# Performance work log

Hardware: AMD Instinct MI355X
Metric: run time of the kernel (lower is better)

## Reference

```python
import jax, jax.numpy as jnp
import numpy as np

INPUT_SIZE = 64
OUTPUT_SIZE = 64
HIDDEN = 1024
SAMPLES = 32
STEPS = 128


def _forward(inputs, W_in, b_in, W_ih0, W_hh0, b_ih0, b_hh0,
             W_ih1, W_hh1, b_ih1, b_hh1, W_out, b_out):
    # Faithful to the torch module: per outer step, inputs[:, step, :].unsqueeze(1)
    # is fed to a batch_first=False LSTM, so the sample axis acts as time (batch=1)
    # and hidden state carries across steps -> equivalent to ONE batch-1 LSTM over
    # the step-major flattened sequence of length steps*samples.
    # Dropout (p=0.05 between LSTM layers) is treated as eval-mode (identity).
    S, steps, D = inputs.shape
    H = W_in.shape[0]
    x = jnp.transpose(inputs, (1, 0, 2)).reshape(steps * S, D)  # (T, D), step-major
    z = x @ W_in.T + b_in                                        # input Linear (T, H)
    # layer-0 input contributions precomputed over all time (big GEMM)
    pre0 = z @ W_ih0.T + (b_ih0 + b_hh0)                         # (T, 4H)
    b1 = b_ih1 + b_hh1

    def step(carry, p0):
        h0, c0, h1, c1 = carry
        g0 = p0 + W_hh0 @ h0                                      # (4H,)
        i0, f0, gg0, o0 = jnp.split(g0, 4)
        c0 = jax.nn.sigmoid(f0) * c0 + jax.nn.sigmoid(i0) * jnp.tanh(gg0)
        h0 = jax.nn.sigmoid(o0) * jnp.tanh(c0)
        g1 = W_ih1 @ h0 + W_hh1 @ h1 + b1
        i1, f1, gg1, o1 = jnp.split(g1, 4)
        c1 = jax.nn.sigmoid(f1) * c1 + jax.nn.sigmoid(i1) * jnp.tanh(gg1)
        h1 = jax.nn.sigmoid(o1) * jnp.tanh(c1)
        return (h0, c0, h1, c1), h1

    zero = jnp.zeros((H,), inputs.dtype)
    (_, _, _, _), hs = jax.lax.scan(step, (zero, zero, zero, zero), pre0)  # hs: (T, H)
    y = hs @ W_out.T + b_out                                     # output Linear (T, out)
    return jnp.transpose(y.reshape(steps, S, -1), (1, 0, 2))     # (samples, steps, out)


def setup_inputs() -> dict:
    key = jax.random.key(0)
    ks = jax.random.split(key, 16)
    H, D, O = HIDDEN, INPUT_SIZE, OUTPUT_SIZE
    s = 1.0 / np.sqrt(H)
    u = lambda k, shape: jax.random.uniform(k, shape, jnp.float32, -s, s)
    return {
        "inputs": jax.random.normal(ks[0], (SAMPLES, STEPS, D), jnp.float32),
        "W_in": u(ks[1], (H, D)),
        "b_in": u(ks[2], (H,)),
        "W_ih0": u(ks[3], (4 * H, H)),
        "W_hh0": u(ks[4], (4 * H, H)),
        "b_ih0": u(ks[5], (4 * H,)),
        "b_hh0": u(ks[6], (4 * H,)),
        "W_ih1": u(ks[7], (4 * H, H)),
        "W_hh1": u(ks[8], (4 * H, H)),
        "b_ih1": u(ks[9], (4 * H,)),
        "b_hh1": u(ks[10], (4 * H,)),
        "W_out": u(ks[11], (O, H)),
        "b_out": u(ks[12], (O,)),
    }


def reference(inputs, W_in, b_in, W_ih0, W_hh0, b_ih0, b_hh0,
              W_ih1, W_hh1, b_ih1, b_hh1, W_out, b_out):
    return _forward(inputs, W_in, b_in, W_ih0, W_hh0, b_ih0, b_hh0,
                    W_ih1, W_hh1, b_ih1, b_hh1, W_out, b_out)
```

## Files before the change

kernel.cpp:

```cpp
#include <hip/hip_runtime.h>
#include <math.h>


#define T_STEPS 4096
#define HID 1024
#define UPB 8
#define NBLK 256

typedef unsigned long long u64;

#define AGENT_LD64(p) __hip_atomic_load((p), __ATOMIC_RELAXED, __HIP_MEMORY_SCOPE_AGENT)
#define AGENT_ST64(p, v) __hip_atomic_store((p), (v), __ATOMIC_RELAXED, __HIP_MEMORY_SCOPE_AGENT)

__device__ __forceinline__ u64 pack_h(float h, int tag) {
  return (u64)__float_as_uint(h) | ((u64)(unsigned)tag << 32);
}
__device__ __forceinline__ float pkt_val(u64 v) { return __uint_as_float((unsigned)v); }
__device__ __forceinline__ int pkt_tag(u64 v) { return (int)(v >> 32); }

__device__ __forceinline__ float fast_sigm(float x) {
  return __builtin_amdgcn_rcpf(1.f + __expf(-x));
}
__device__ __forceinline__ float fast_tanh(float x) {
  return 2.f * __builtin_amdgcn_rcpf(1.f + __expf(-2.f * x)) - 1.f;
}

__device__ __forceinline__ void pace_wait(u64 t_last, u64 per) {
  if (per) {
    u64 target = t_last + (per >> 1) + (per >> 4);
    while ((long long)(__builtin_amdgcn_s_memrealtime() - target) < 0)
      __builtin_amdgcn_s_sleep(2);
  }
}
__device__ __forceinline__ void pace_update(u64* t_last, u64* per) {
  u64 now = __builtin_amdgcn_s_memrealtime();
  if (*t_last) {
    u64 d = now - *t_last;
    if (d > 1024) d = 1024;
    *per = *per ? ((*per * 3 + d) >> 2) : d;
  }
  *t_last = now;
}

__global__ void k_clear(u64* __restrict__ p, long n) {
  long i = (long)blockIdx.x * blockDim.x + threadIdx.x;
  long stride = (long)gridDim.x * blockDim.x;
  for (; i < n; i += stride) p[i] = 0ULL;
}

__global__ void k_prep(const float* __restrict__ inputs,
                       const float* __restrict__ b_ih0, const float* __restrict__ b_hh0,
                       const float* __restrict__ b_ih1, const float* __restrict__ b_hh1,
                       float* __restrict__ xg, float* __restrict__ bsum0,
                       float* __restrict__ b1sum) {
  int i = blockIdx.x * 256 + threadIdx.x;
  if (i < T_STEPS * 64) {
    int t = i >> 6, d = i & 63;
    xg[i] = inputs[(t & 31) * 8192 + (t >> 5) * 64 + d];
  }
  if (i < 4096) {
    bsum0[i] = b_ih0[i] + b_hh0[i];
    b1sum[i] = b_ih1[i] + b_hh1[i];
  }
}

__global__ __launch_bounds__(256) void gemm_nt(
    const float* __restrict__ A, const float* __restrict__ B,
    const float* __restrict__ bias, float* __restrict__ C,
    int M, int N, int K, int mode) {
  __shared__ float As[8][128];
  __shared__ float Bs[8][128];
  const int tid = threadIdx.x;
  const int bm = blockIdx.x * 128;
  const int bn = blockIdx.y * 128;
  const int tm = tid >> 4;
  const int tn = tid & 15;
  const int lr = tid >> 1;
  const int lk = (tid & 1) * 4;

  float acc[8][8];
#pragma unroll
  for (int i = 0; i < 8; i++)
#pragma unroll
    for (int j = 0; j < 8; j++) acc[i][j] = 0.f;

  const float* Ap = A + (long)(bm + lr) * K + lk;
  const bool bvalid = (bn + lr) < N;
  const float* Bp = B + (long)(bvalid ? (bn + lr) : 0) * K + lk;

  for (int k0 = 0; k0 < K; k0 += 8) {
    float4 av = *(const float4*)(Ap + k0);
    float4 bv = bvalid ? *(const float4*)(Bp + k0) : make_float4(0.f, 0.f, 0.f, 0.f);
    As[lk + 0][lr] = av.x; As[lk + 1][lr] = av.y;
    As[lk + 2][lr] = av.z; As[lk + 3][lr] = av.w;
    Bs[lk + 0][lr] = bv.x; Bs[lk + 1][lr] = bv.y;
    Bs[lk + 2][lr] = bv.z; Bs[lk + 3][lr] = bv.w;
    __syncthreads();
#pragma unroll
    for (int kk = 0; kk < 8; kk++) {
      float a[8], b[8];
      *(float4*)&a[0] = *(const float4*)&As[kk][tm * 8];
      *(float4*)&a[4] = *(const float4*)&As[kk][tm * 8 + 4];
      *(float4*)&b[0] = *(const float4*)&Bs[kk][tn * 8];
      *(float4*)&b[4] = *(const float4*)&Bs[kk][tn * 8 + 4];
#pragma unroll
      for (int i = 0; i < 8; i++)
#pragma unroll
        for (int j = 0; j < 8; j++) acc[i][j] = fmaf(a[i], b[j], acc[i][j]);
    }
    __syncthreads();
  }

  const int n0 = bn + tn * 8;
  if (n0 < N) {
    float bb[8];
#pragma unroll
    for (int j = 0; j < 8; j++) bb[j] = bias[n0 + j];
#pragma unroll
    for (int i = 0; i < 8; i++) {
      int m = bm + tm * 8 + i;
      float4 v0, v1;
      v0.x = acc[i][0] + bb[0]; v0.y = acc[i][1] + bb[1];
      v0.z = acc[i][2] + bb[2]; v0.w = acc[i][3] + bb[3];
      v1.x = acc[i][4] + bb[4]; v1.y = acc[i][5] + bb[5];
      v1.z = acc[i][6] + bb[6]; v1.w = acc[i][7] + bb[7];
      if (mode == 0) {
        long o = (long)m * N + n0;
        *(float4*)&C[o] = v0; *(float4*)&C[o + 4] = v1;
      } else {
        long o = (long)(m & 31) * 8192 + (long)(m >> 5) * 64 + n0;
        *(float4*)&C[o] = v0; *(float4*)&C[o + 4] = v1;
      }
    }
  }
}

__global__ __launch_bounds__(1024, 1) void lstm_fused(
    const float* __restrict__ pre0,
    const float* __restrict__ Whh0,
    const float* __restrict__ Wih1,
    const float* __restrict__ Whh1,
    const float* __restrict__ b1sum,
    u64* __restrict__ pk0,
    u64* __restrict__ pk1,
    float* __restrict__ h1_hist) {
  __shared__ float ha_lds[HID];
  __shared__ float hb_lds[HID];
  __shared__ float scr[32];
  __shared__ float pre_lds[32];
  const int b = blockIdx.x;
  const int tid = threadIdx.x;
  const int wave = tid >> 6;
  const int lane = tid & 63;

  if (b < 128) {
    const int j0 = b * UPB;
    float w0[16], w1[16];
    {
      int r0 = 2 * wave, r1 = 2 * wave + 1;
      const float* s0 = Whh0 + (long)((r0 >> 3) * HID + j0 + (r0 & 7)) * HID + lane;
      const float* s1 = Whh0 + (long)((r1 >> 3) * HID + j0 + (r1 & 7)) * HID + lane;
#pragma unroll
      for (int m = 0; m < 16; m++) { w0[m] = s0[m << 6]; w1[m] = s1[m << 6]; }
    }
    float c_state = 0.f;
    u64 t_last = 0, per = 0;
    __syncthreads();

    for (int t = 0; t < T_STEPS; t++) {
      float preval = 0.f;
      if (tid < 32)
        preval = pre0[(long)t * 4096 + ((tid >> 3) << 10) + j0 + (tid & 7)];

      if (t > 0) {
        const u64* p = pk0 + (long)(t - 1) * HID + tid;
        pace_wait(t_last, per);
        u64 v;
        for (;;) {
          v = AGENT_LD64(p);
          if (pkt_tag(v) == t) break;
          __builtin_amdgcn_s_sleep(1);
        }
        pace_update(&t_last, &per);
        ha_lds[tid] = pkt_val(v);
      } else {
        ha_lds[tid] = 0.f;
      }
      if (tid < 32) pre_lds[tid] = preval;
      __syncthreads();

      float s0 = 0.f, s1 = 0.f;
#pragma unroll
      for (int m = 0; m < 16; m++) {
        float hv = ha_lds[lane + (m << 6)];
        s0 = fmaf(w0[m], hv, s0);
        s1 = fmaf(w1[m], hv, s1);
      }
#pragma unroll
      for (int off = 32; off >= 1; off >>= 1) {
        s0 += __shfl_xor(s0, off, 64);
        s1 += __shfl_xor(s1, off, 64);
      }
      if (lane == 0) { scr[wave * 2] = s0; scr[wave * 2 + 1] = s1; }
      __syncthreads();

      if (tid < UPB) {
        float gi = scr[tid]      + pre_lds[tid];
        float gf = scr[8 + tid]  + pre_lds[8 + tid];
        float gg = scr[16 + tid] + pre_lds[16 + tid];
        float go = scr[24 + tid] + pre_lds[24 + tid];
        c_state = fast_sigm(gf) * c_state + fast_sigm(gi) * fast_tanh(gg);
        float h = fast_sigm(go) * fast_tanh(c_state);
        AGENT_ST64(&pk0[(long)t * HID + j0 + tid], pack_h(h, t + 1));
      }
    }
  } else {
    const int j0 = (b - 128) * UPB;
    float wi0[16], wi1[16], wh0[16], wh1[16];
    {
      int r0 = 2 * wave, r1 = 2 * wave + 1;
      long o0 = (long)((r0 >> 3) * HID + j0 + (r0 & 7)) * HID + lane;
      long o1 = (long)((r1 >> 3) * HID + j0 + (r1 & 7)) * HID + lane;
      const float* a0 = Wih1 + o0; const float* a1 = Wih1 + o1;
      const float* c0 = Whh1 + o0; const float* c1 = Whh1 + o1;
#pragma unroll
      for (int m = 0; m < 16; m++) {
        wi0[m] = a0[m << 6]; wi1[m] = a1[m << 6];
        wh0[m] = c0[m << 6]; wh1[m] = c1[m << 6];
      }
    }
    if (tid < 32)
      pre_lds[tid] = b1sum[((tid >> 3) << 10) + j0 + (tid & 7)];
    float c_state = 0.f;
    u64 t_last = 0, per = 0;
    __syncthreads();

    for (int r = 1; r <= T_STEPS; r++) {
      const u64* p0 = pk0 + (long)(r - 1) * HID + tid;
      const u64* p1 = pk1 + (long)((r >= 2) ? (r - 2) : 0) * HID + tid;
      pace_wait(t_last, per);
      u64 v0 = 0, v1 = 0;
      bool ok0 = false, ok1 = (r < 2);
      for (;;) {
        if (!ok0) { v0 = AGENT_LD64(p0); ok0 = (pkt_tag(v0) == r); }
        if (!ok1) { v1 = AGENT_LD64(p1); ok1 = (pkt_tag(v1) == r - 1); }
        if (ok0 && ok1) break;
        __builtin_amdgcn_s_sleep(1);
      }
      pace_update(&t_last, &per);
      ha_lds[tid] = pkt_val(v0);
      hb_lds[tid] = (r >= 2) ? pkt_val(v1) : 0.f;
      __syncthreads();

      float s0 = 0.f, s1 = 0.f;
#pragma unroll
      for (int m = 0; m < 16; m++) {
        float av = ha_lds[lane + (m << 6)];
        float bv = hb_lds[lane + (m << 6)];
        s0 = fmaf(wi0[m], av, s0);
        s0 = fmaf(wh0[m], bv, s0);
        s1 = fmaf(wi1[m], av, s1);
        s1 = fmaf(wh1[m], bv, s1);
      }
#pragma unroll
      for (int off = 32; off >= 1; off >>= 1) {
        s0 += __shfl_xor(s0, off, 64);
        s1 += __shfl_xor(s1, off, 64);
      }
      if (lane == 0) { scr[wave * 2] = s0; scr[wave * 2 + 1] = s1; }
      __syncthreads();

      if (tid < UPB) {
        float gi = scr[tid]      + pre_lds[tid];
        float gf = scr[8 + tid]  + pre_lds[8 + tid];
        float gg = scr[16 + tid] + pre_lds[16 + tid];
        float go = scr[24 + tid] + pre_lds[24 + tid];
        c_state = fast_sigm(gf) * c_state + fast_sigm(gi) * fast_tanh(gg);
        float h = fast_sigm(go) * fast_tanh(c_state);
        AGENT_ST64(&pk1[(long)(r - 1) * HID + j0 + tid], pack_h(h, r));
        h1_hist[(long)(r - 1) * HID + j0 + tid] = h;
      }
    }
  }
}

extern "C" void kernel_launch(void* const* d_in, const int* in_sizes, int n_in,
                              void* d_out, int out_size, void* d_ws, size_t ws_size,
                              hipStream_t stream) {
  const float* inputs = (const float*)d_in[0];
  const float* W_in  = (const float*)d_in[1];
  const float* b_in  = (const float*)d_in[2];
  const float* W_ih0 = (const float*)d_in[3];
  const float* W_hh0 = (const float*)d_in[4];
  const float* b_ih0 = (const float*)d_in[5];
  const float* b_hh0 = (const float*)d_in[6];
  const float* W_ih1 = (const float*)d_in[7];
  const float* W_hh1 = (const float*)d_in[8];
  const float* b_ih1 = (const float*)d_in[9];
  const float* b_hh1 = (const float*)d_in[10];
  const float* W_out = (const float*)d_in[11];
  const float* b_out = (const float*)d_in[12];
  float* out = (float*)d_out;

  char* ws = (char*)d_ws;
  float* pre_big = (float*)(ws);
  u64*   pk0     = (u64*)  (ws + ((size_t)64 << 20));
  u64*   pk1     = (u64*)  (ws + ((size_t)96 << 20));
  float* zbuf    = (float*)(ws + ((size_t)128 << 20));
  float* xg      = (float*)(ws + ((size_t)144 << 20));
  float* bsum0   = (float*)(ws + ((size_t)145 << 20));
  float* b1sum   = (float*)(ws + ((size_t)145 << 20) + 16384);

  k_clear<<<2048, 256, 0, stream>>>(pk0, (long)2 * T_STEPS * HID);
  k_prep<<<1024, 256, 0, stream>>>(inputs, b_ih0, b_hh0, b_ih1, b_hh1,
                                   xg, bsum0, b1sum);
  gemm_nt<<<dim3(32, 8), 256, 0, stream>>>(xg, W_in, b_in, zbuf,
                                           T_STEPS, HID, 64, 0);
  gemm_nt<<<dim3(32, 32), 256, 0, stream>>>(zbuf, W_ih0, bsum0, pre_big,
                                            T_STEPS, 4096, HID, 0);
  lstm_fused<<<NBLK, 1024, 0, stream>>>(pre_big, W_hh0, W_ih1, W_hh1, b1sum,
                                        pk0, pk1, zbuf);
  gemm_nt<<<dim3(32, 1), 256, 0, stream>>>(zbuf, W_out, b_out, out,
                                           T_STEPS, 64, HID, 1);
}
```

Before: 10.27 ms.

## Remap LSTM recurrence to one hidden unit per wave with single barrier per step

Result: slower. 18.13 ms (+76.6%).

```diff
diff --git a/kernel.cpp b/kernel.cpp
--- a/kernel.cpp
+++ b/kernel.cpp
@@ -27,7 +27,7 @@
 
 __device__ __forceinline__ void pace_wait(u64 t_last, u64 per) {
   if (per) {
-    u64 target = t_last + (per >> 1) + (per >> 4);
+    u64 target = t_last + (per >> 2) + (per >> 3);
     while ((long long)(__builtin_amdgcn_s_memrealtime() - target) < 0)
       __builtin_amdgcn_s_sleep(2);
   }
@@ -135,7 +135,7 @@
   }
 }
 
-__global__ __launch_bounds__(1024, 1) void lstm_fused(
+__global__ __launch_bounds__(512) void lstm_fused(
     const float* __restrict__ pre0,
     const float* __restrict__ Whh0,
     const float* __restrict__ Wih1,
@@ -144,141 +144,164 @@
     u64* __restrict__ pk0,
     u64* __restrict__ pk1,
     float* __restrict__ h1_hist) {
-  __shared__ float ha_lds[HID];
-  __shared__ float hb_lds[HID];
-  __shared__ float scr[32];
-  __shared__ float pre_lds[32];
+  __shared__ float ha[2][HID];
+  __shared__ float hb[2][HID];
   const int b = blockIdx.x;
   const int tid = threadIdx.x;
   const int wave = tid >> 6;
   const int lane = tid & 63;
 
   if (b < 128) {
-    const int j0 = b * UPB;
-    float w0[16], w1[16];
-    {
-      int r0 = 2 * wave, r1 = 2 * wave + 1;
-      const float* s0 = Whh0 + (long)((r0 >> 3) * HID + j0 + (r0 & 7)) * HID + lane;
-      const float* s1 = Whh0 + (long)((r1 >> 3) * HID + j0 + (r1 & 7)) * HID + lane;
-#pragma unroll
-      for (int m = 0; m < 16; m++) { w0[m] = s0[m << 6]; w1[m] = s1[m << 6]; }
-    }
+    const int u = b * UPB + wave;
+    float4 wgt[4][4];
+#pragma unroll
+    for (int g = 0; g < 4; g++)
+#pragma unroll
+      for (int q = 0; q < 4; q++)
+        wgt[g][q] = *(const float4*)(Whh0 + ((long)((g << 10) + u) << 10) +
+                                     (q << 8) + (lane << 2));
     float c_state = 0.f;
     u64 t_last = 0, per = 0;
-    __syncthreads();
 
     for (int t = 0; t < T_STEPS; t++) {
       float preval = 0.f;
-      if (tid < 32)
-        preval = pre0[(long)t * 4096 + ((tid >> 3) << 10) + j0 + (tid & 7)];
+      if (lane < 4) preval = pre0[(long)t * 4096 + (lane << 10) + u];
+      const int par = t & 1;
 
       if (t > 0) {
-        const u64* p = pk0 + (long)(t - 1) * HID + tid;
+        const u64* p = pk0 + (long)(t - 1) * HID + 2 * tid;
         pace_wait(t_last, per);
-        u64 v;
+        u64 v0, v1;
         for (;;) {
-          v = AGENT_LD64(p);
-          if (pkt_tag(v) == t) break;
+          v0 = AGENT_LD64(p); v1 = AGENT_LD64(p + 1);
+          if (pkt_tag(v0) == t && pkt_tag(v1) == t) break;
           __builtin_amdgcn_s_sleep(1);
         }
         pace_update(&t_last, &per);
-        ha_lds[tid] = pkt_val(v);
+        *(float2*)&ha[par][2 * tid] = make_float2(pkt_val(v0), pkt_val(v1));
       } else {
-        ha_lds[tid] = 0.f;
-      }
-      if (tid < 32) pre_lds[tid] = preval;
+        *(float2*)&ha[par][2 * tid] = make_float2(0.f, 0.f);
+      }
       __syncthreads();
 
-      float s0 = 0.f, s1 = 0.f;
-#pragma unroll
-      for (int m = 0; m < 16; m++) {
-        float hv = ha_lds[lane + (m << 6)];
-        s0 = fmaf(w0[m], hv, s0);
-        s1 = fmaf(w1[m], hv, s1);
+      float s0 = 0.f, s1 = 0.f, s2 = 0.f, s3 = 0.f;
+#pragma unroll
+      for (int q = 0; q < 4; q++) {
+        float4 hv = *(const float4*)&ha[par][(q << 8) + (lane << 2)];
+        s0 = fmaf(wgt[0][q].x, hv.x, s0); s0 = fmaf(wgt[0][q].y, hv.y, s0);
+        s0 = fmaf(wgt[0][q].z, hv.z, s0); s0 = fmaf(wgt[0][q].w, hv.w, s0);
+        s1 = fmaf(wgt[1][q].x, hv.x, s1); s1 = fmaf(wgt[1][q].y, hv.y, s1);
+        s1 = fmaf(wgt[1][q].z, hv.z, s1); s1 = fmaf(wgt[1][q].w, hv.w, s1);
+        s2 = fmaf(wgt[2][q].x, hv.x, s2); s2 = fmaf(wgt[2][q].y, hv.y, s2);
+        s2 = fmaf(wgt[2][q].z, hv.z, s2); s2 = fmaf(wgt[2][q].w, hv.w, s2);
+        s3 = fmaf(wgt[3][q].x, hv.x, s3); s3 = fmaf(wgt[3][q].y, hv.y, s3);
+        s3 = fmaf(wgt[3][q].z, hv.z, s3); s3 = fmaf(wgt[3][q].w, hv.w, s3);
       }
 #pragma unroll
       for (int off = 32; off >= 1; off >>= 1) {
-        s0 += __shfl_xor(s0, off, 64);
-        s1 += __shfl_xor(s1, off, 64);
-      }
-      if (lane == 0) { scr[wave * 2] = s0; scr[wave * 2 + 1] = s1; }
-      __syncthreads();
-
-      if (tid < UPB) {
-        float gi = scr[tid]      + pre_lds[tid];
-        float gf = scr[8 + tid]  + pre_lds[8 + tid];
-        float gg = scr[16 + tid] + pre_lds[16 + tid];
-        float go = scr[24 + tid] + pre_lds[24 + tid];
-        c_state = fast_sigm(gf) * c_state + fast_sigm(gi) * fast_tanh(gg);
-        float h = fast_sigm(go) * fast_tanh(c_state);
-        AGENT_ST64(&pk0[(long)t * HID + j0 + tid], pack_h(h, t + 1));
+        s0 += __shfl_xor(s0, off, 64); s1 += __shfl_xor(s1, off, 64);
+        s2 += __shfl_xor(s2, off, 64); s3 += __shfl_xor(s3, off, 64);
+      }
+      float act = 0.f;
+      if (lane < 4) {
+        float sel = (lane == 0) ? s0 : (lane == 1) ? s1 : (lane == 2) ? s2 : s3;
+        sel += preval;
+        act = (lane == 2) ? fast_tanh(sel) : fast_sigm(sel);
+      }
+      float af = __shfl(act, 1, 64);
+      float ag = __shfl(act, 2, 64);
+      float ao = __shfl(act, 3, 64);
+      if (lane == 0) {
+        c_state = af * c_state + act * ag;
+        float h = ao * fast_tanh(c_state);
+        AGENT_ST64(&pk0[(long)t * HID + u], pack_h(h, t + 1));
       }
     }
   } else {
-    const int j0 = (b - 128) * UPB;
-    float wi0[16], wi1[16], wh0[16], wh1[16];
-    {
-      int r0 = 2 * wave, r1 = 2 * wave + 1;
-      long o0 = (long)((r0 >> 3) * HID + j0 + (r0 & 7)) * HID + lane;
-      long o1 = (long)((r1 >> 3) * HID + j0 + (r1 & 7)) * HID + lane;
-      const float* a0 = Wih1 + o0; const float* a1 = Wih1 + o1;
-      const float* c0 = Whh1 + o0; const float* c1 = Whh1 + o1;
-#pragma unroll
-      for (int m = 0; m < 16; m++) {
-        wi0[m] = a0[m << 6]; wi1[m] = a1[m << 6];
-        wh0[m] = c0[m << 6]; wh1[m] = c1[m << 6];
-      }
-    }
-    if (tid < 32)
-      pre_lds[tid] = b1sum[((tid >> 3) << 10) + j0 + (tid & 7)];
+    const int u = (b - 128) * UPB + wave;
+    float4 wi[4][4], wh[4][4];
+#pragma unroll
+    for (int g = 0; g < 4; g++)
+#pragma unroll
+      for (int q = 0; q < 4; q++) {
+        long o = ((long)((g << 10) + u) << 10) + (q << 8) + (lane << 2);
+        wi[g][q] = *(const float4*)(Wih1 + o);
+        wh[g][q] = *(const float4*)(Whh1 + o);
+      }
+    float preval = 0.f;
+    if (lane < 4) preval = b1sum[(lane << 10) + u];
     float c_state = 0.f;
     u64 t_last = 0, per = 0;
-    __syncthreads();
 
     for (int r = 1; r <= T_STEPS; r++) {
-      const u64* p0 = pk0 + (long)(r - 1) * HID + tid;
-      const u64* p1 = pk1 + (long)((r >= 2) ? (r - 2) : 0) * HID + tid;
+      const int par = r & 1;
+      const u64* p0 = pk0 + (long)(r - 1) * HID + 2 * tid;
+      const u64* p1 = pk1 + (long)((r >= 2) ? (r - 2) : 0) * HID + 2 * tid;
       pace_wait(t_last, per);
-      u64 v0 = 0, v1 = 0;
-      bool ok0 = false, ok1 = (r < 2);
-      for (;;) {
-        if (!ok0) { v0 = AGENT_LD64(p0); ok0 = (pkt_tag(v0) == r); }
-        if (!ok1) { v1 = AGENT_LD64(p1); ok1 = (pkt_tag(v1) == r - 1); }
-        if (ok0 && ok1) break;
-        __builtin_amdgcn_s_sleep(1);
+      u64 a0, a1, b0 = 0, b1 = 0;
+      if (r >= 2) {
+        for (;;) {
+          a0 = AGENT_LD64(p0); a1 = AGENT_LD64(p0 + 1);
+          b0 = AGENT_LD64(p1); b1 = AGENT_LD64(p1 + 1);
+          if (pkt_tag(a0) == r && pkt_tag(a1) == r &&
+              pkt_tag(b0) == r - 1 && pkt_tag(b1) == r - 1) break;
+          __builtin_amdgcn_s_sleep(1);
+        }
+      } else {
+        for (;;) {
+          a0 = AGENT_LD64(p0); a1 = AGENT_LD64(p0 + 1);
+          if (pkt_tag(a0) == r && pkt_tag(a1) == r) break;
+          __builtin_amdgcn_s_sleep(1);
+        }
       }
       pace_update(&t_last, &per);
-      ha_lds[tid] = pkt_val(v0);
-      hb_lds[tid] = (r >= 2) ? pkt_val(v1) : 0.f;
+      *(float2*)&ha[par][2 * tid] = make_float2(pkt_val(a0), pkt_val(a1));
+      *(float2*)&hb[par][2 * tid] = (r >= 2)
+          ? make_float2(pkt_val(b0), pkt_val(b1))
+          : make_float2(0.f, 0.f);
       __syncthreads();
 
-      float s0 = 0.f, s1 = 0.f;
-#pragma unroll
-      for (int m = 0; m < 16; m++) {
-        float av = ha_lds[lane + (m << 6)];
-        float bv = hb_lds[lane + (m << 6)];
-        s0 = fmaf(wi0[m], av, s0);
-        s0 = fmaf(wh0[m], bv, s0);
-        s1 = fmaf(wi1[m], av, s1);
-        s1 = fmaf(wh1[m], bv, s1);
+      float s0 = 0.f, s1 = 0.f, s2 = 0.f, s3 = 0.f;
+#pragma unroll
+      for (int q = 0; q < 4; q++) {
+        float4 va = *(const float4*)&ha[par][(q << 8) + (lane << 2)];
+        float4 vb = *(const float4*)&hb[par][(q << 8) + (lane << 2)];
+        s0 = fmaf(wi[0][q].x, va.x, s0); s0 = fmaf(wi[0][q].y, va.y, s0);
+        s0 = fmaf(wi[0][q].z, va.z, s0); s0 = fmaf(wi[0][q].w, va.w, s0);
+        s0 = fmaf(wh[0][q].x, vb.x, s0); s0 = fmaf(wh[0][q].y, vb.y, s0);
+        s0 = fmaf(wh[0][q].z, vb.z, s0); s0 = fmaf(wh[0][q].w, vb.w, s0);
+        s1 = fmaf(wi[1][q].x, va.x, s1); s1 = fmaf(wi[1][q].y, va.y, s1);
+        s1 = fmaf(wi[1][q].z, va.z, s1); s1 = fmaf(wi[1][q].w, va.w, s1);
+        s1 = fmaf(wh[1][q].x, vb.x, s1); s1 = fmaf(wh[1][q].y, vb.y, s1);
+        s1 = fmaf(wh[1][q].z, vb.z, s1); s1 = fmaf(wh[1][q].w, vb.w, s1);
+        s2 = fmaf(wi[2][q].x, va.x, s2); s2 = fmaf(wi[2][q].y, va.y, s2);
+        s2 = fmaf(wi[2][q].z, va.z, s2); s2 = fmaf(wi[2][q].w, va.w, s2);
+        s2 = fmaf(wh[2][q].x, vb.x, s2); s2 = fmaf(wh[2][q].y, vb.y, s2);
+        s2 = fmaf(wh[2][q].z, vb.z, s2); s2 = fmaf(wh[2][q].w, vb.w, s2);
+        s3 = fmaf(wi[3][q].x, va.x, s3); s3 = fmaf(wi[3][q].y, va.y, s3);
+        s3 = fmaf(wi[3][q].z, va.z, s3); s3 = fmaf(wi[3][q].w, va.w, s3);
+        s3 = fmaf(wh[3][q].x, vb.x, s3); s3 = fmaf(wh[3][q].y, vb.y, s3);
+        s3 = fmaf(wh[3][q].z, vb.z, s3); s3 = fmaf(wh[3][q].w, vb.w, s3);
       }
 #pragma unroll
       for (int off = 32; off >= 1; off >>= 1) {
-        s0 += __shfl_xor(s0, off, 64);
-        s1 += __shfl_xor(s1, off, 64);
-      }
-      if (lane == 0) { scr[wave * 2] = s0; scr[wave * 2 + 1] = s1; }
-      __syncthreads();
-
-      if (tid < UPB) {
-        float gi = scr[tid]      + pre_lds[tid];
-        float gf = scr[8 + tid]  + pre_lds[8 + tid];
-        float gg = scr[16 + tid] + pre_lds[16 + tid];
-        float go = scr[24 + tid] + pre_lds[24 + tid];
-        c_state = fast_sigm(gf) * c_state + fast_sigm(gi) * fast_tanh(gg);
-        float h = fast_sigm(go) * fast_tanh(c_state);
-        AGENT_ST64(&pk1[(long)(r - 1) * HID + j0 + tid], pack_h(h, r));
-        h1_hist[(long)(r - 1) * HID + j0 + tid] = h;
+        s0 += __shfl_xor(s0, off, 64); s1 += __shfl_xor(s1, off, 64);
+        s2 += __shfl_xor(s2, off, 64); s3 += __shfl_xor(s3, off, 64);
+      }
+      float act = 0.f;
+      if (lane < 4) {
+        float sel = (lane == 0) ? s0 : (lane == 1) ? s1 : (lane == 2) ? s2 : s3;
+        sel += preval;
+        act = (lane == 2) ? fast_tanh(sel) : fast_sigm(sel);
+      }
+      float af = __shfl(act, 1, 64);
+      float ag = __shfl(act, 2, 64);
+      float ao = __shfl(act, 3, 64);
+      if (lane == 0) {
+        c_state = af * c_state + act * ag;
+        float h = ao * fast_tanh(c_state);
+        AGENT_ST64(&pk1[(long)(r - 1) * HID + u], pack_h(h, r));
+        h1_hist[(long)(r - 1) * HID + u] = h;
       }
     }
   }
@@ -318,8 +341,8 @@
                                            T_STEPS, HID, 64, 0);
   gemm_nt<<<dim3(32, 32), 256, 0, stream>>>(zbuf, W_ih0, bsum0, pre_big,
                                             T_STEPS, 4096, HID, 0);
-  lstm_fused<<<NBLK, 1024, 0, stream>>>(pre_big, W_hh0, W_ih1, W_hh1, b1sum,
-                                        pk0, pk1, zbuf);
+  lstm_fused<<<NBLK, 512, 0, stream>>>(pre_big, W_hh0, W_ih1, W_hh1, b1sum,
+                                       pk0, pk1, zbuf);
   gemm_nt<<<dim3(32, 1), 256, 0, stream>>>(zbuf, W_out, b_out, out,
                                            T_STEPS, 64, HID, 1);
 }
```

## Merge both LSTM layers into every block with 4 units per block

Applied to the files above, without the earlier changes.

Result: slower. 16.68 ms (+62.5%).

```diff
diff --git a/kernel.cpp b/kernel.cpp
--- a/kernel.cpp
+++ b/kernel.cpp
@@ -4,7 +4,7 @@
 
 #define T_STEPS 4096
 #define HID 1024
-#define UPB 8
+#define UPB 4
 #define NBLK 256
 
 typedef unsigned long long u64;
@@ -27,7 +27,7 @@
 
 __device__ __forceinline__ void pace_wait(u64 t_last, u64 per) {
   if (per) {
-    u64 target = t_last + (per >> 1) + (per >> 4);
+    u64 target = t_last + (per >> 1);
     while ((long long)(__builtin_amdgcn_s_memrealtime() - target) < 0)
       __builtin_amdgcn_s_sleep(2);
   }
@@ -135,7 +135,7 @@
   }
 }
 
-__global__ __launch_bounds__(1024, 1) void lstm_fused(
+__global__ __launch_bounds__(1024) void lstm_fused(
     const float* __restrict__ pre0,
     const float* __restrict__ Whh0,
     const float* __restrict__ Wih1,
@@ -144,141 +144,135 @@
     u64* __restrict__ pk0,
     u64* __restrict__ pk1,
     float* __restrict__ h1_hist) {
-  __shared__ float ha_lds[HID];
-  __shared__ float hb_lds[HID];
-  __shared__ float scr[32];
-  __shared__ float pre_lds[32];
+  __shared__ float ha[2][HID];
+  __shared__ float hb[2][HID];
+  __shared__ float scr0[4][16];
+  __shared__ float scr1[4][16];
   const int b = blockIdx.x;
   const int tid = threadIdx.x;
   const int wave = tid >> 6;
   const int lane = tid & 63;
-
-  if (b < 128) {
-    const int j0 = b * UPB;
-    float w0[16], w1[16];
-    {
-      int r0 = 2 * wave, r1 = 2 * wave + 1;
-      const float* s0 = Whh0 + (long)((r0 >> 3) * HID + j0 + (r0 & 7)) * HID + lane;
-      const float* s1 = Whh0 + (long)((r1 >> 3) * HID + j0 + (r1 & 7)) * HID + lane;
-#pragma unroll
-      for (int m = 0; m < 16; m++) { w0[m] = s0[m << 6]; w1[m] = s1[m << 6]; }
-    }
-    float c_state = 0.f;
-    u64 t_last = 0, per = 0;
-    __syncthreads();
-
-    for (int t = 0; t < T_STEPS; t++) {
-      float preval = 0.f;
-      if (tid < 32)
-        preval = pre0[(long)t * 4096 + ((tid >> 3) << 10) + j0 + (tid & 7)];
-
-      if (t > 0) {
-        const u64* p = pk0 + (long)(t - 1) * HID + tid;
-        pace_wait(t_last, per);
-        u64 v;
-        for (;;) {
-          v = AGENT_LD64(p);
-          if (pkt_tag(v) == t) break;
-          __builtin_amdgcn_s_sleep(1);
-        }
-        pace_update(&t_last, &per);
-        ha_lds[tid] = pkt_val(v);
-      } else {
-        ha_lds[tid] = 0.f;
-      }
-      if (tid < 32) pre_lds[tid] = preval;
-      __syncthreads();
-
-      float s0 = 0.f, s1 = 0.f;
-#pragma unroll
-      for (int m = 0; m < 16; m++) {
-        float hv = ha_lds[lane + (m << 6)];
-        s0 = fmaf(w0[m], hv, s0);
-        s1 = fmaf(w1[m], hv, s1);
-      }
-#pragma unroll
-      for (int off = 32; off >= 1; off >>= 1) {
-        s0 += __shfl_xor(s0, off, 64);
-        s1 += __shfl_xor(s1, off, 64);
-      }
-      if (lane == 0) { scr[wave * 2] = s0; scr[wave * 2 + 1] = s1; }
-      __syncthreads();
-
-      if (tid < UPB) {
-        float gi = scr[tid]      + pre_lds[tid];
-        float gf = scr[8 + tid]  + pre_lds[8 + tid];
-        float gg = scr[16 + tid] + pre_lds[16 + tid];
-        float go = scr[24 + tid] + pre_lds[24 + tid];
-        c_state = fast_sigm(gf) * c_state + fast_sigm(gi) * fast_tanh(gg);
-        float h = fast_sigm(go) * fast_tanh(c_state);
-        AGENT_ST64(&pk0[(long)t * HID + j0 + tid], pack_h(h, t + 1));
-      }
-    }
-  } else {
-    const int j0 = (b - 128) * UPB;
-    float wi0[16], wi1[16], wh0[16], wh1[16];
-    {
-      int r0 = 2 * wave, r1 = 2 * wave + 1;
-      long o0 = (long)((r0 >> 3) * HID + j0 + (r0 & 7)) * HID + lane;
-      long o1 = (long)((r1 >> 3) * HID + j0 + (r1 & 7)) * HID + lane;
-      const float* a0 = Wih1 + o0; const float* a1 = Wih1 + o1;
-      const float* c0 = Whh1 + o0; const float* c1 = Whh1 + o1;
-#pragma unroll
-      for (int m = 0; m < 16; m++) {
-        wi0[m] = a0[m << 6]; wi1[m] = a1[m << 6];
-        wh0[m] = c0[m << 6]; wh1[m] = c1[m << 6];
-      }
-    }
-    if (tid < 32)
-      pre_lds[tid] = b1sum[((tid >> 3) << 10) + j0 + (tid & 7)];
-    float c_state = 0.f;
-    u64 t_last = 0, per = 0;
-    __syncthreads();
-
-    for (int r = 1; r <= T_STEPS; r++) {
-      const u64* p0 = pk0 + (long)(r - 1) * HID + tid;
-      const u64* p1 = pk1 + (long)((r >= 2) ? (r - 2) : 0) * HID + tid;
+  const int lu = wave & 3;
+  const int kq = wave >> 2;
+  const int u0 = b * UPB;
+  const int tg = lane >> 2;
+  const int tlu = lane & 3;
+
+  float w0[4][4], wi[4][4], wh[4][4];
+#pragma unroll
+  for (int g = 0; g < 4; g++) {
+    const long off = (((long)(g << 10) + u0 + lu) << 10) + (kq << 8) + lane;
+#pragma unroll
+    for (int m = 0; m < 4; m++) {
+      w0[g][m] = Whh0[off + (m << 6)];
+      wi[g][m] = Wih1[off + (m << 6)];
+      wh[g][m] = Whh1[off + (m << 6)];
+    }
+  }
+  float b1v = 0.f;
+  if (wave == 1 && lane < 16) b1v = b1sum[(tg << 10) + u0 + tlu];
+  float c0 = 0.f;
+  float c1 = 0.f;
+  u64 t_last = 0, per = 0;
+
+  for (int t = 0; t <= T_STEPS; t++) {
+    const int par = t & 1;
+    float preval = 0.f;
+    if (wave == 0 && lane < 16 && t < T_STEPS)
+      preval = pre0[(long)t * 4096 + (tg << 10) + u0 + tlu];
+
+    if (t > 0) {
+      const u64* p0 = pk0 + (((long)(t - 1)) << 10) + tid;
+      const u64* p1 = pk1 + (((long)((t >= 2) ? (t - 2) : 0)) << 10) + tid;
       pace_wait(t_last, per);
       u64 v0 = 0, v1 = 0;
-      bool ok0 = false, ok1 = (r < 2);
+      bool ok0 = false, ok1 = (t < 2);
       for (;;) {
-        if (!ok0) { v0 = AGENT_LD64(p0); ok0 = (pkt_tag(v0) == r); }
-        if (!ok1) { v1 = AGENT_LD64(p1); ok1 = (pkt_tag(v1) == r - 1); }
+        if (!ok0) { v0 = AGENT_LD64(p0); ok0 = (pkt_tag(v0) == t); }
+        if (!ok1) { v1 = AGENT_LD64(p1); ok1 = (pkt_tag(v1) == t - 1); }
         if (ok0 && ok1) break;
         __builtin_amdgcn_s_sleep(1);
       }
       pace_update(&t_last, &per);
-      ha_lds[tid] = pkt_val(v0);
-      hb_lds[tid] = (r >= 2) ? pkt_val(v1) : 0.f;
-      __syncthreads();
-
-      float s0 = 0.f, s1 = 0.f;
-#pragma unroll
-      for (int m = 0; m < 16; m++) {
-        float av = ha_lds[lane + (m << 6)];
-        float bv = hb_lds[lane + (m << 6)];
-        s0 = fmaf(wi0[m], av, s0);
-        s0 = fmaf(wh0[m], bv, s0);
-        s1 = fmaf(wi1[m], av, s1);
-        s1 = fmaf(wh1[m], bv, s1);
+      ha[par][tid] = pkt_val(v0);
+      hb[par][tid] = (t >= 2) ? pkt_val(v1) : 0.f;
+    } else {
+      ha[0][tid] = 0.f;
+      hb[0][tid] = 0.f;
+    }
+    __syncthreads();
+
+    if (t < T_STEPS) {
+      float s0 = 0.f, s1 = 0.f, s2 = 0.f, s3 = 0.f;
+      const float* hap = &ha[par][(kq << 8) + lane];
+#pragma unroll
+      for (int m = 0; m < 4; m++) {
+        float hv = hap[m << 6];
+        s0 = fmaf(w0[0][m], hv, s0); s1 = fmaf(w0[1][m], hv, s1);
+        s2 = fmaf(w0[2][m], hv, s2); s3 = fmaf(w0[3][m], hv, s3);
       }
 #pragma unroll
       for (int off = 32; off >= 1; off >>= 1) {
-        s0 += __shfl_xor(s0, off, 64);
-        s1 += __shfl_xor(s1, off, 64);
-      }
-      if (lane == 0) { scr[wave * 2] = s0; scr[wave * 2 + 1] = s1; }
-      __syncthreads();
-
-      if (tid < UPB) {
-        float gi = scr[tid]      + pre_lds[tid];
-        float gf = scr[8 + tid]  + pre_lds[8 + tid];
-        float gg = scr[16 + tid] + pre_lds[16 + tid];
-        float go = scr[24 + tid] + pre_lds[24 + tid];
-        c_state = fast_sigm(gf) * c_state + fast_sigm(gi) * fast_tanh(gg);
-        float h = fast_sigm(go) * fast_tanh(c_state);
-        AGENT_ST64(&pk1[(long)(r - 1) * HID + j0 + tid], pack_h(h, r));
-        h1_hist[(long)(r - 1) * HID + j0 + tid] = h;
+        s0 += __shfl_xor(s0, off, 64); s1 += __shfl_xor(s1, off, 64);
+        s2 += __shfl_xor(s2, off, 64); s3 += __shfl_xor(s3, off, 64);
+      }
+      if (lane < 4) {
+        float v = (lane == 0) ? s0 : (lane == 1) ? s1 : (lane == 2) ? s2 : s3;
+        scr0[kq][(lane << 2) + lu] = v;
+      }
+    }
+    __syncthreads();
+
+    if (wave == 0 && lane < 16 && t < T_STEPS) {
+      float sum = scr0[0][lane] + scr0[1][lane] + scr0[2][lane] +
+                  scr0[3][lane] + preval;
+      float a = (tg == 2) ? fast_tanh(sum) : fast_sigm(sum);
+      float af = __shfl(a, 4 + tlu, 64);
+      float ag = __shfl(a, 8 + tlu, 64);
+      float ao = __shfl(a, 12 + tlu, 64);
+      if (lane < 4) {
+        c0 = af * c0 + a * ag;
+        float h = ao * fast_tanh(c0);
+        AGENT_ST64(&pk0[((long)t << 10) + u0 + lane], pack_h(h, t + 1));
+      }
+    }
+    if (t >= 1) {
+      float s0 = 0.f, s1 = 0.f, s2 = 0.f, s3 = 0.f;
+      const float* hap = &ha[par][(kq << 8) + lane];
+      const float* hbp = &hb[par][(kq << 8) + lane];
+#pragma unroll
+      for (int m = 0; m < 4; m++) {
+        float av = hap[m << 6];
+        float bv = hbp[m << 6];
+        s0 = fmaf(wi[0][m], av, s0); s0 = fmaf(wh[0][m], bv, s0);
+        s1 = fmaf(wi[1][m], av, s1); s1 = fmaf(wh[1][m], bv, s1);
+        s2 = fmaf(wi[2][m], av, s2); s2 = fmaf(wh[2][m], bv, s2);
+        s3 = fmaf(wi[3][m], av, s3); s3 = fmaf(wh[3][m], bv, s3);
+      }
+#pragma unroll
+      for (int off = 32; off >= 1; off >>= 1) {
+        s0 += __shfl_xor(s0, off, 64); s1 += __shfl_xor(s1, off, 64);
+        s2 += __shfl_xor(s2, off, 64); s3 += __shfl_xor(s3, off, 64);
+      }
+      if (lane < 4) {
+        float v = (lane == 0) ? s0 : (lane == 1) ? s1 : (lane == 2) ? s2 : s3;
+        scr1[kq][(lane << 2) + lu] = v;
+      }
+    }
+    __syncthreads();
+
+    if (wave == 1 && lane < 16 && t >= 1) {
+      float sum = scr1[0][lane] + scr1[1][lane] + scr1[2][lane] +
+                  scr1[3][lane] + b1v;
+      float a = (tg == 2) ? fast_tanh(sum) : fast_sigm(sum);
+      float af = __shfl(a, 4 + tlu, 64);
+      float ag = __shfl(a, 8 + tlu, 64);
+      float ao = __shfl(a, 12 + tlu, 64);
+      if (lane < 4) {
+        c1 = af * c1 + a * ag;
+        float h = ao * fast_tanh(c1);
+        AGENT_ST64(&pk1[((long)(t - 1) << 10) + u0 + lane], pack_h(h, t));
+        h1_hist[((long)(t - 1) << 10) + u0 + lane] = h;
       }
     }
   }
```

## Precompute layer-1 input projection off the critical path and parallelize gate activations

Applied to the files above, without the earlier changes.

New measurement: 9.972 ms. 1.03x faster.

```diff
diff --git a/kernel.cpp b/kernel.cpp
--- a/kernel.cpp
+++ b/kernel.cpp
@@ -27,7 +27,7 @@
 
 __device__ __forceinline__ void pace_wait(u64 t_last, u64 per) {
   if (per) {
-    u64 target = t_last + (per >> 1) + (per >> 4);
+    u64 target = t_last + (per >> 1);
     while ((long long)(__builtin_amdgcn_s_memrealtime() - target) < 0)
       __builtin_amdgcn_s_sleep(2);
   }
@@ -147,7 +147,6 @@
   __shared__ float ha_lds[HID];
   __shared__ float hb_lds[HID];
   __shared__ float scr[32];
-  __shared__ float pre_lds[32];
   const int b = blockIdx.x;
   const int tid = threadIdx.x;
   const int wave = tid >> 6;
@@ -186,7 +185,6 @@
       } else {
         ha_lds[tid] = 0.f;
       }
-      if (tid < 32) pre_lds[tid] = preval;
       __syncthreads();
 
       float s0 = 0.f, s1 = 0.f;
@@ -204,14 +202,17 @@
       if (lane == 0) { scr[wave * 2] = s0; scr[wave * 2 + 1] = s1; }
       __syncthreads();
 
-      if (tid < UPB) {
-        float gi = scr[tid]      + pre_lds[tid];
-        float gf = scr[8 + tid]  + pre_lds[8 + tid];
-        float gg = scr[16 + tid] + pre_lds[16 + tid];
-        float go = scr[24 + tid] + pre_lds[24 + tid];
-        c_state = fast_sigm(gf) * c_state + fast_sigm(gi) * fast_tanh(gg);
-        float h = fast_sigm(go) * fast_tanh(c_state);
-        AGENT_ST64(&pk0[(long)t * HID + j0 + tid], pack_h(h, t + 1));
+      if (tid < 32) {
+        float sum = scr[tid] + preval;
+        float a = ((tid >> 3) == 2) ? fast_tanh(sum) : fast_sigm(sum);
+        float af = __shfl(a,  8 + (tid & 7), 64);
+        float ag = __shfl(a, 16 + (tid & 7), 64);
+        float ao = __shfl(a, 24 + (tid & 7), 64);
+        if (tid < 8) {
+          c_state = af * c_state + a * ag;
+          float h = ao * fast_tanh(c_state);
+          AGENT_ST64(&pk0[(long)t * HID + j0 + tid], pack_h(h, t + 1));
+        }
       }
     }
   } else {
@@ -229,37 +230,53 @@
         wh0[m] = c0[m << 6]; wh1[m] = c1[m << 6];
       }
     }
-    if (tid < 32)
-      pre_lds[tid] = b1sum[((tid >> 3) << 10) + j0 + (tid & 7)];
+    float b1v = 0.f;
+    if (tid < 32) b1v = b1sum[((tid >> 3) << 10) + j0 + (tid & 7)];
     float c_state = 0.f;
     u64 t_last = 0, per = 0;
     __syncthreads();
 
-    for (int r = 1; r <= T_STEPS; r++) {
-      const u64* p0 = pk0 + (long)(r - 1) * HID + tid;
-      const u64* p1 = pk1 + (long)((r >= 2) ? (r - 2) : 0) * HID + tid;
-      pace_wait(t_last, per);
-      u64 v0 = 0, v1 = 0;
-      bool ok0 = false, ok1 = (r < 2);
+    float sA0 = 0.f, sA1 = 0.f;
+    {
+      const u64* p = pk0 + tid;
+      u64 v;
       for (;;) {
-        if (!ok0) { v0 = AGENT_LD64(p0); ok0 = (pkt_tag(v0) == r); }
-        if (!ok1) { v1 = AGENT_LD64(p1); ok1 = (pkt_tag(v1) == r - 1); }
-        if (ok0 && ok1) break;
+        v = AGENT_LD64(p);
+        if (pkt_tag(v) == 1) break;
         __builtin_amdgcn_s_sleep(1);
       }
-      pace_update(&t_last, &per);
-      ha_lds[tid] = pkt_val(v0);
-      hb_lds[tid] = (r >= 2) ? pkt_val(v1) : 0.f;
-      __syncthreads();
-
-      float s0 = 0.f, s1 = 0.f;
+      ha_lds[tid] = pkt_val(v);
+      __syncthreads();
 #pragma unroll
       for (int m = 0; m < 16; m++) {
         float av = ha_lds[lane + (m << 6)];
+        sA0 = fmaf(wi0[m], av, sA0);
+        sA1 = fmaf(wi1[m], av, sA1);
+      }
+    }
+
+    for (int r = 1; r <= T_STEPS; r++) {
+      if (r >= 2) {
+        const u64* p = pk1 + (long)(r - 2) * HID + tid;
+        pace_wait(t_last, per);
+        u64 v;
+        for (;;) {
+          v = AGENT_LD64(p);
+          if (pkt_tag(v) == r - 1) break;
+          __builtin_amdgcn_s_sleep(1);
+        }
+        pace_update(&t_last, &per);
+        hb_lds[tid] = pkt_val(v);
+      } else {
+        hb_lds[tid] = 0.f;
+      }
+      __syncthreads();
+
+      float s0 = sA0, s1 = sA1;
+#pragma unroll
+      for (int m = 0; m < 16; m++) {
         float bv = hb_lds[lane + (m << 6)];
-        s0 = fmaf(wi0[m], av, s0);
         s0 = fmaf(wh0[m], bv, s0);
-        s1 = fmaf(wi1[m], av, s1);
         s1 = fmaf(wh1[m], bv, s1);
       }
 #pragma unroll
@@ -270,15 +287,38 @@
       if (lane == 0) { scr[wave * 2] = s0; scr[wave * 2 + 1] = s1; }
       __syncthreads();
 
-      if (tid < UPB) {
-        float gi = scr[tid]      + pre_lds[tid];
-        float gf = scr[8 + tid]  + pre_lds[8 + tid];
-        float gg = scr[16 + tid] + pre_lds[16 + tid];
-        float go = scr[24 + tid] + pre_lds[24 + tid];
-        c_state = fast_sigm(gf) * c_state + fast_sigm(gi) * fast_tanh(gg);
-        float h = fast_sigm(go) * fast_tanh(c_state);
-        AGENT_ST64(&pk1[(long)(r - 1) * HID + j0 + tid], pack_h(h, r));
-        h1_hist[(long)(r - 1) * HID + j0 + tid] = h;
+      if (tid < 32) {
+        float sum = scr[tid] + b1v;
+        float a = ((tid >> 3) == 2) ? fast_tanh(sum) : fast_sigm(sum);
+        float af = __shfl(a,  8 + (tid & 7), 64);
+        float ag = __shfl(a, 16 + (tid & 7), 64);
+        float ao = __shfl(a, 24 + (tid & 7), 64);
+        if (tid < 8) {
+          c_state = af * c_state + a * ag;
+          float h = ao * fast_tanh(c_state);
+          AGENT_ST64(&pk1[(long)(r - 1) * HID + j0 + tid], pack_h(h, r));
+          h1_hist[(long)(r - 1) * HID + j0 + tid] = h;
+        }
+      }
+
+      if (r < T_STEPS) {
+        const u64* p = pk0 + (long)r * HID + tid;
+        u64 v;
+        for (;;) {
+          v = AGENT_LD64(p);
+          if (pkt_tag(v) == r + 1) break;
+          __builtin_amdgcn_s_sleep(1);
+        }
+        ha_lds[tid] = pkt_val(v);
+        __syncthreads();
+        float n0 = 0.f, n1 = 0.f;
+#pragma unroll
+        for (int m = 0; m < 16; m++) {
+          float av = ha_lds[lane + (m << 6)];
+          n0 = fmaf(wi0[m], av, n0);
+          n1 = fmaf(wi1[m], av, n1);
+        }
+        sA0 = n0; sA1 = n1;
       }
     }
   }
```
